# Kernel tuning notes

Measured on AMD Instinct MI355X. Metric: run time of the kernel, lower is better.

## Reference

```python
import jax, jax.numpy as jnp
import numpy as np

D_MODEL = 1024
D_STATE = 16
D_CONV = 4
EXPAND = 2
DT_RANK = 64
D_INNER = EXPAND * D_MODEL  # 2048
BATCH = 2
SEQ = 1024


def _silu(v):
    return v * jax.nn.sigmoid(v)


def setup_inputs() -> dict:
    key = jax.random.key(0)
    ks = jax.random.split(key, 8)
    x = jax.random.normal(ks[0], (BATCH, SEQ, D_MODEL), dtype=jnp.float32)
    W_in = jax.random.normal(ks[1], (2 * D_INNER, D_MODEL), dtype=jnp.float32) * (D_MODEL ** -0.5)
    conv_w = jax.random.normal(ks[2], (D_INNER, 1, D_CONV), dtype=jnp.float32) * (D_CONV ** -0.5)
    conv_b = jnp.zeros((D_INNER,), dtype=jnp.float32)
    W_x = jax.random.normal(ks[3], (DT_RANK + 2 * D_STATE, D_INNER), dtype=jnp.float32) * (D_INNER ** -0.5)
    W_dt = jax.random.uniform(ks[4], (D_INNER, DT_RANK), minval=-(DT_RANK ** -0.5), maxval=DT_RANK ** -0.5, dtype=jnp.float32)
    # dt bias init: inverse-softplus of dt sampled log-uniform in [1e-3, 1e-1]
    dt = jnp.exp(jax.random.uniform(ks[5], (D_INNER,), dtype=jnp.float32) * (np.log(0.1) - np.log(0.001)) + np.log(0.001))
    dt = jnp.clip(dt, 1e-4)
    b_dt = dt + jnp.log(-jnp.expm1(-dt))
    # A_log init: log of 1..d_state tiled per channel (S4D-real)
    A_log = jnp.log(jnp.tile(jnp.arange(1, D_STATE + 1, dtype=jnp.float32), (D_INNER, 1)))
    D = jnp.ones((D_INNER,), dtype=jnp.float32)
    W_out = jax.random.normal(ks[6], (D_MODEL, D_INNER), dtype=jnp.float32) * (D_INNER ** -0.5)
    return {"x": x, "W_in": W_in, "conv_w": conv_w, "conv_b": conv_b, "W_x": W_x,
            "W_dt": W_dt, "b_dt": b_dt, "A_log": A_log, "D": D, "W_out": W_out}


def _selective_scan(u, dt, A, B_in, C_in, D):
    # u, dt: [B,L,d_inner]; B_in, C_in: [B,L,d_state]; A: [d_inner,d_state]; D: [d_inner]
    Bsz = u.shape[0]

    def step(h, inp):
        u_t, dt_t, B_t, C_t = inp  # [B,d_inner], [B,d_inner], [B,d_state], [B,d_state]
        dA = jnp.exp(dt_t[:, :, None] * A)                     # [B,d_inner,d_state]
        h = dA * h + dt_t[:, :, None] * B_t[:, None, :] * u_t[:, :, None]
        y = jnp.einsum('bds,bs->bd', h, C_t)
        return h, y

    h0 = jnp.zeros((Bsz, D_INNER, D_STATE), dtype=u.dtype)
    xs = (u.transpose(1, 0, 2), dt.transpose(1, 0, 2),
          B_in.transpose(1, 0, 2), C_in.transpose(1, 0, 2))
    _, ys = jax.lax.scan(step, h0, xs)                          # ys: [L,B,d_inner]
    return ys.transpose(1, 0, 2) + u * D


def reference(x, W_in, conv_w, conv_b, W_x, W_dt, b_dt, A_log, D, W_out):
    # in_proj and gate split
    xz = x @ W_in.T                                            # [B,T,2*d_inner]
    x_in, z = jnp.split(xz, 2, axis=-1)
    # depthwise causal conv1d (left-pad d_conv-1, same as pad-both + slice :T)
    xi = x_in.transpose(0, 2, 1)                               # [B,d_inner,T]
    conv = jax.lax.conv_general_dilated(xi, conv_w, window_strides=(1,),
                                        padding=[(D_CONV - 1, 0)],
                                        feature_group_count=D_INNER)
    x_act = _silu(conv + conv_b[None, :, None]).transpose(0, 2, 1)  # [B,T,d_inner]
    # dt / B / C projections
    dbc = x_act @ W_x.T
    dt_lr, B_in, C_in = jnp.split(dbc, [DT_RANK, DT_RANK + D_STATE], axis=-1)
    dt = jax.nn.softplus(dt_lr @ W_dt.T + b_dt)                # [B,T,d_inner]
    A = -jnp.exp(A_log)                                        # [d_inner,d_state]
    y = _selective_scan(x_act, dt, A, B_in, C_in, D)
    y = y * _silu(z)
    return y @ W_out.T
```

## Files before the change

kernel.cpp:

```cpp
#include <hip/hip_runtime.h>
#include <math.h>

#define D_MODEL 1024
#define D_STATE 16
#define D_CONV  4
#define DT_RANK 64
#define D_INNER 2048
#define BATCH   2
#define SEQ     1024
#define BT      (BATCH*SEQ)
#define NCHUNK  32
#define CLEN    (SEQ/NCHUNK)
#define KSPLIT  16

typedef int   v4i __attribute__((ext_vector_type(4)));
typedef float v4f __attribute__((ext_vector_type(4)));
typedef unsigned short u16;

template<int BM, int BN, int BK, int TM, int TN, int EPI>
__launch_bounds__(256)
__global__ void gemm_nt(const float* __restrict__ A, int lda,
                        const float* __restrict__ B, int ldb,
                        float* __restrict__ C, int ldc,
                        int K, const float* __restrict__ bias) {
    constexpr int BX = BN / TN;
    constexpr int BY = BM / TM;
    constexpr int THREADS = BX * BY;

    __shared__ float As[BK][BM + 1];
    __shared__ float Bs[BK][BN + 1];

    const int tid = threadIdx.x;
    const int tx  = tid % BX;
    const int ty  = tid / BX;
    const int m0  = blockIdx.y * BM;
    const int n0  = blockIdx.x * BN;

    float acc[TM][TN] = {};

    for (int k0 = 0; k0 < K; k0 += BK) {
        #pragma unroll
        for (int l = 0; l < (BM * BK) / (THREADS * 4); ++l) {
            int idx = (tid + l * THREADS) * 4;
            int row = idx / BK, col = idx % BK;
            const float4 v = *reinterpret_cast<const float4*>(
                &A[(size_t)(m0 + row) * lda + k0 + col]);
            As[col + 0][row] = v.x; As[col + 1][row] = v.y;
            As[col + 2][row] = v.z; As[col + 3][row] = v.w;
        }
        #pragma unroll
        for (int l = 0; l < (BN * BK) / (THREADS * 4); ++l) {
            int idx = (tid + l * THREADS) * 4;
            int row = idx / BK, col = idx % BK;
            const float4 v = *reinterpret_cast<const float4*>(
                &B[(size_t)(n0 + row) * ldb + k0 + col]);
            Bs[col + 0][row] = v.x; Bs[col + 1][row] = v.y;
            Bs[col + 2][row] = v.z; Bs[col + 3][row] = v.w;
        }
        __syncthreads();

        #pragma unroll
        for (int kk = 0; kk < BK; ++kk) {
            float a[TM], b[TN];
            #pragma unroll
            for (int i = 0; i < TM; ++i) a[i] = As[kk][ty * TM + i];
            #pragma unroll
            for (int j = 0; j < TN; ++j) b[j] = Bs[kk][tx * TN + j];
            #pragma unroll
            for (int i = 0; i < TM; ++i)
                #pragma unroll
                for (int j = 0; j < TN; ++j)
                    acc[i][j] = fmaf(a[i], b[j], acc[i][j]);
        }
        __syncthreads();
    }

    #pragma unroll
    for (int i = 0; i < TM; ++i) {
        float* outp = &C[(size_t)(m0 + ty * TM + i) * ldc + n0 + tx * TN];
        float vals[4];
        #pragma unroll
        for (int j = 0; j < TN; ++j) {
            float val = acc[i][j];
            if (EPI == 1) {
                val += bias[n0 + tx * TN + j];
                val = (val > 20.f) ? val : log1pf(expf(val));
            }
            vals[j] = val;
        }
        float4 v;
        v.x = vals[0]; v.y = vals[1]; v.z = vals[2]; v.w = vals[3];
        *reinterpret_cast<float4*>(outp) = v;
    }
}

template<int BM, int BN, int BK, int TM, int TN>
__launch_bounds__(128)
__global__ void gemm_nt_splitk(const float* __restrict__ A, int lda,
                               const float* __restrict__ B, int ldb,
                               float* __restrict__ part, int N, int kchunk) {
    constexpr int BX = BN / TN;
    constexpr int BY = BM / TM;
    constexpr int THREADS = BX * BY;

    __shared__ float As[BK][BM + 1];
    __shared__ float Bs[BK][BN + 1];

    const int tid = threadIdx.x;
    const int tx  = tid % BX;
    const int ty  = tid / BX;
    const int m0  = blockIdx.y * BM;
    const int n0  = blockIdx.x * BN;
    const int kb  = blockIdx.z * kchunk;

    float acc[TM][TN] = {};

    for (int k0 = kb; k0 < kb + kchunk; k0 += BK) {
        #pragma unroll
        for (int l = 0; l < (BM * BK) / (THREADS * 4); ++l) {
            int idx = (tid + l * THREADS) * 4;
            int row = idx / BK, col = idx % BK;
            const float4 v = *reinterpret_cast<const float4*>(
                &A[(size_t)(m0 + row) * lda + k0 + col]);
            As[col + 0][row] = v.x; As[col + 1][row] = v.y;
            As[col + 2][row] = v.z; As[col + 3][row] = v.w;
        }
        #pragma unroll
        for (int l = 0; l < (BN * BK) / (THREADS * 4); ++l) {
            int idx = (tid + l * THREADS) * 4;
            int row = idx / BK, col = idx % BK;
            const float4 v = *reinterpret_cast<const float4*>(
                &B[(size_t)(n0 + row) * ldb + k0 + col]);
            Bs[col + 0][row] = v.x; Bs[col + 1][row] = v.y;
            Bs[col + 2][row] = v.z; Bs[col + 3][row] = v.w;
        }
        __syncthreads();

        #pragma unroll
        for (int kk = 0; kk < BK; ++kk) {
            float a[TM], b[TN];
            #pragma unroll
            for (int i = 0; i < TM; ++i) a[i] = As[kk][ty * TM + i];
            #pragma unroll
            for (int j = 0; j < TN; ++j) b[j] = Bs[kk][tx * TN + j];
            #pragma unroll
            for (int i = 0; i < TM; ++i)
                #pragma unroll
                for (int j = 0; j < TN; ++j)
                    acc[i][j] = fmaf(a[i], b[j], acc[i][j]);
        }
        __syncthreads();
    }

    float* base = part + (size_t)blockIdx.z * BT * N;
    #pragma unroll
    for (int i = 0; i < TM; ++i) {
        float* outp = &base[(size_t)(m0 + ty * TM + i) * N + n0 + tx * TN];
        float4 v;
        v.x = acc[i][0]; v.y = acc[i][1]; v.z = acc[i][2]; v.w = acc[i][3];
        *reinterpret_cast<float4*>(outp) = v;
    }
}

__global__ void reduce_splitk(const float* __restrict__ part,
                              float* __restrict__ outp, int n) {
    const int idx = blockIdx.x * 256 + threadIdx.x;
    if (idx >= n) return;
    float s = 0.f;
    #pragma unroll
    for (int kc = 0; kc < KSPLIT; ++kc)
        s += part[(size_t)kc * n + idx];
    outp[idx] = s;
}

__device__ __forceinline__ u16 rne_bf16(float x) {
    unsigned int u = __float_as_uint(x);
    unsigned int r = u + 0x7FFFu + ((u >> 16) & 1u);
    return (u16)(r >> 16);
}

__global__ void prep_kernel(const float* __restrict__ x,
                            const float* __restrict__ Win,
                            const float* __restrict__ Wout,
                            u16* __restrict__ xhi, u16* __restrict__ xlo,
                            u16* __restrict__ winh, u16* __restrict__ wouth) {
    const size_t M2 = 2u * 1024u * 1024u;
    size_t i = ((size_t)blockIdx.x * 256 + threadIdx.x) * 8;
    if (i < M2) {
        float4 a = *reinterpret_cast<const float4*>(&x[i]);
        float4 b = *reinterpret_cast<const float4*>(&x[i + 4]);
        float xs[8] = {a.x, a.y, a.z, a.w, b.x, b.y, b.z, b.w};
        unsigned int hw[4], lw[4];
        #pragma unroll
        for (int q = 0; q < 4; ++q) {
            u16 h0 = rne_bf16(xs[2*q]);
            u16 h1 = rne_bf16(xs[2*q+1]);
            float d0 = xs[2*q]   - __uint_as_float((unsigned int)h0 << 16);
            float d1 = xs[2*q+1] - __uint_as_float((unsigned int)h1 << 16);
            hw[q] = (unsigned int)h0 | ((unsigned int)h1 << 16);
            lw[q] = (unsigned int)rne_bf16(d0) | ((unsigned int)rne_bf16(d1) << 16);
        }
        *reinterpret_cast<v4i*>(&xhi[i]) = *reinterpret_cast<v4i*>(hw);
        *reinterpret_cast<v4i*>(&xlo[i]) = *reinterpret_cast<v4i*>(lw);
    } else if (i < 3 * M2) {
        size_t j = i - M2;
        float4 a = *reinterpret_cast<const float4*>(&Win[j]);
        float4 b = *reinterpret_cast<const float4*>(&Win[j + 4]);
        float xs[8] = {a.x, a.y, a.z, a.w, b.x, b.y, b.z, b.w};
        unsigned int hw[4];
        #pragma unroll
        for (int q = 0; q < 4; ++q)
            hw[q] = (unsigned int)rne_bf16(xs[2*q]) | ((unsigned int)rne_bf16(xs[2*q+1]) << 16);
        *reinterpret_cast<v4i*>(&winh[j]) = *reinterpret_cast<v4i*>(hw);
    } else {
        size_t j = i - 3 * M2;
        float4 a = *reinterpret_cast<const float4*>(&Wout[j]);
        float4 b = *reinterpret_cast<const float4*>(&Wout[j + 4]);
        float xs[8] = {a.x, a.y, a.z, a.w, b.x, b.y, b.z, b.w};
        unsigned int hw[4];
        #pragma unroll
        for (int q = 0; q < 4; ++q)
            hw[q] = (unsigned int)rne_bf16(xs[2*q]) | ((unsigned int)rne_bf16(xs[2*q+1]) << 16);
        *reinterpret_cast<v4i*>(&wouth[j]) = *reinterpret_cast<v4i*>(hw);
    }
}

#define MFMA_B16(ACC, Af, Bf) \
    asm("v_mfma_f32_16x16x32_bf16 %0, %1, %2, %0" : "+v"(ACC) : "v"(Af), "v"(Bf))

template<int BM, int BN, int WM, int WN>
__launch_bounds__(256)
__global__ void gemm_mfma2(const u16* __restrict__ Ahi, const u16* __restrict__ Alo, int lda,
                           const u16* __restrict__ Bhi, int ldb,
                           float* __restrict__ C, int ldc, int K) {
    constexpr int ACH = BM / 64;
    constexpr int BCH = BN / 64;
    constexpr int WMF = WM / 16;
    constexpr int WNF = WN / 16;
    constexpr int SA  = BM * 40;
    constexpr int SB  = BN * 40;
    constexpr int BUFSZ = 2 * SA + SB;
    constexpr int WCOLS = BN / WN;

    __shared__ u16 smem[2 * BUFSZ];

    const int tid  = threadIdx.x;
    const int lane = tid & 63;
    const int wave = tid >> 6;
    const int wr   = wave / WCOLS, wc = wave % WCOLS;
    const int m0   = blockIdx.y * BM, n0 = blockIdx.x * BN;

    size_t aBase[ACH]; int aW[ACH];
    #pragma unroll
    for (int q = 0; q < ACH; ++q) {
        int c = tid + q * 256, row = c >> 2, slot = c & 3;
        aBase[q] = (size_t)(m0 + row) * lda + slot * 8;
        aW[q] = row * 40 + slot * 8;
    }
    size_t bBase[BCH]; int bW[BCH];
    #pragma unroll
    for (int q = 0; q < BCH; ++q) {
        int c = tid + q * 256, row = c >> 2, slot = c & 3;
        bBase[q] = (size_t)(n0 + row) * ldb + slot * 8;
        bW[q] = row * 40 + slot * 8;
    }

    const int fr = lane & 15;
    const int fk = (lane >> 4) * 8;
    const int fq = lane >> 4;
    int aOff[WMF], bOff[WNF];
    #pragma unroll
    for (int i = 0; i < WMF; ++i) aOff[i] = (wr * WM + i * 16 + fr) * 40 + fk;
    #pragma unroll
    for (int j = 0; j < WNF; ++j) bOff[j] = (wc * WN + j * 16 + fr) * 40 + fk;

    v4f acc[WMF][WNF];
    #pragma unroll
    for (int i = 0; i < WMF; ++i)
        #pragma unroll
        for (int j = 0; j < WNF; ++j)
            acc[i][j] = (v4f)0.f;

    v4i rAh[ACH], rAl[ACH], rBh[BCH];
    #pragma unroll
    for (int q = 0; q < ACH; ++q) {
        rAh[q] = *reinterpret_cast<const v4i*>(Ahi + aBase[q]);
        rAl[q] = *reinterpret_cast<const v4i*>(Alo + aBase[q]);
    }
    #pragma unroll
    for (int q = 0; q < BCH; ++q)
        rBh[q] = *reinterpret_cast<const v4i*>(Bhi + bBase[q]);
    #pragma unroll
    for (int q = 0; q < ACH; ++q) {
        *reinterpret_cast<v4i*>(&smem[aW[q]]) = rAh[q];
        *reinterpret_cast<v4i*>(&smem[SA + aW[q]]) = rAl[q];
    }
    #pragma unroll
    for (int q = 0; q < BCH; ++q)
        *reinterpret_cast<v4i*>(&smem[2 * SA + bW[q]]) = rBh[q];
    __syncthreads();

    const int NK = K / 32;
    for (int k = 0; k < NK; ++k) {
        u16* sc = smem + (k & 1) * BUFSZ;
        if (k + 1 < NK) {
            const int k0 = (k + 1) * 32;
            #pragma unroll
            for (int q = 0; q < ACH; ++q) {
                rAh[q] = *reinterpret_cast<const v4i*>(Ahi + aBase[q] + k0);
                rAl[q] = *reinterpret_cast<const v4i*>(Alo + aBase[q] + k0);
            }
            #pragma unroll
            for (int q = 0; q < BCH; ++q)
                rBh[q] = *reinterpret_cast<const v4i*>(Bhi + bBase[q] + k0);
        }

        v4i ah[WMF], al[WMF];
        #pragma unroll
        for (int i = 0; i < WMF; ++i) {
            ah[i] = *reinterpret_cast<const v4i*>(&sc[aOff[i]]);
            al[i] = *reinterpret_cast<const v4i*>(&sc[SA + aOff[i]]);
        }
        #pragma unroll
        for (int j = 0; j < WNF; ++j) {
            v4i bh = *reinterpret_cast<const v4i*>(&sc[2 * SA + bOff[j]]);
            #pragma unroll
            for (int i = 0; i < WMF; ++i) {
                MFMA_B16(acc[i][j], ah[i], bh);
                MFMA_B16(acc[i][j], al[i], bh);
            }
        }

        if (k + 1 < NK) {
            u16* sn = smem + ((k + 1) & 1) * BUFSZ;
            #pragma unroll
            for (int q = 0; q < ACH; ++q) {
                *reinterpret_cast<v4i*>(&sn[aW[q]]) = rAh[q];
                *reinterpret_cast<v4i*>(&sn[SA + aW[q]]) = rAl[q];
            }
            #pragma unroll
            for (int q = 0; q < BCH; ++q)
                *reinterpret_cast<v4i*>(&sn[2 * SA + bW[q]]) = rBh[q];
            __syncthreads();
        }
    }

    asm volatile("s_nop 7\n\ts_nop 7\n\ts_nop 7" ::: "memory");

    #pragma unroll
    for (int i = 0; i < WMF; ++i) {
        const int row = m0 + wr * WM + i * 16 + fq * 4;
        #pragma unroll
        for (int j = 0; j < WNF; ++j) {
            const int col = n0 + wc * WN + j * 16 + fr;
            #pragma unroll
            for (int r = 0; r < 4; ++r)
                C[(size_t)(row + r) * ldc + col] = acc[i][j][r];
        }
    }
}

__global__ void conv_silu_kernel(const float* __restrict__ x_in, int xld,
                                 const float* __restrict__ w,
                                 const float* __restrict__ b,
                                 float* __restrict__ x_act) {
    const int idx = blockIdx.x * blockDim.x + threadIdx.x;
    const int ch = idx % D_INNER;
    const int m  = idx / D_INNER;
    const int t  = m % SEQ;

    float acc = b[ch];
    #pragma unroll
    for (int j = 0; j < D_CONV; ++j) {
        int tt = t - (D_CONV - 1) + j;
        if (tt >= 0)
            acc = fmaf(w[ch * D_CONV + j], x_in[(size_t)(m - (D_CONV - 1) + j) * xld + ch], acc);
    }
    x_act[idx] = acc / (1.f + __expf(-acc));
}

__launch_bounds__(256)
__global__ void scan_part1(const float* __restrict__ dt,
                           const float* __restrict__ x_act,
                           const float* __restrict__ dbc,
                           const float* __restrict__ A_log,
                           float* __restrict__ P, float* __restrict__ F) {
    __shared__ float Bsh[CLEN][D_STATE];
    const int tid = threadIdx.x;
    const int d = blockIdx.x * 256 + tid;
    const int c = blockIdx.y;
    const int b = blockIdx.z;
    const int mbase = b * SEQ + c * CLEN;

    {
        const int s = tid & 15, t0 = tid >> 4;
        #pragma unroll
        for (int q = 0; q < 2; ++q)
            Bsh[t0 + 16 * q][s] = dbc[(size_t)(mbase + t0 + 16 * q) * 96 + DT_RANK + s];
    }
    float A[16];
    #pragma unroll
    for (int q = 0; q < 4; ++q) {
        float4 v = *reinterpret_cast<const float4*>(&A_log[d * 16 + q * 4]);
        A[q*4+0] = -__expf(v.x); A[q*4+1] = -__expf(v.y);
        A[q*4+2] = -__expf(v.z); A[q*4+3] = -__expf(v.w);
    }
    __syncthreads();

    float h[16] = {};
    float Pp[16];
    #pragma unroll
    for (int s = 0; s < 16; ++s) Pp[s] = 1.f;

    for (int t = 0; t < CLEN; ++t) {
        const int m = mbase + t;
        const float dtv = dt[(size_t)m * D_INNER + d];
        const float u   = x_act[(size_t)m * D_INNER + d];
        const float du  = dtv * u;
        float Bv[16];
        #pragma unroll
        for (int q = 0; q < 4; ++q) {
            float4 v = *reinterpret_cast<const float4*>(&Bsh[t][q * 4]);
            Bv[q*4+0] = v.x; Bv[q*4+1] = v.y; Bv[q*4+2] = v.z; Bv[q*4+3] = v.w;
        }
        #pragma unroll
        for (int s = 0; s < 16; ++s) {
            const float dA = __expf(dtv * A[s]);
            Pp[s] *= dA;
            h[s] = fmaf(dA, h[s], du * Bv[s]);
        }
    }
    const size_t base = ((size_t)(b * NCHUNK + c) * 16) * D_INNER + d;
    #pragma unroll
    for (int s = 0; s < 16; ++s) {
        P[base + (size_t)s * D_INNER] = Pp[s];
        F[base + (size_t)s * D_INNER] = h[s];
    }
}

__launch_bounds__(256, 2)
__global__ void scan_combine(const float* __restrict__ P, float* F) {
    const int idx = blockIdx.x * 256 + threadIdx.x;
    const int d  = idx % D_INNER;
    const int bs = idx / D_INNER;
    const int b  = bs >> 4, s = bs & 15;
    const size_t base0 = ((size_t)b * NCHUNK * 16 + s) * D_INNER + d;
    const size_t cstep = (size_t)16 * D_INNER;

    float Pv[NCHUNK], Fv[NCHUNK];
    #pragma unroll
    for (int c = 0; c < NCHUNK; ++c) {
        Pv[c] = P[base0 + c * cstep];
        Fv[c] = F[base0 + c * cstep];
    }
    float G = 0.f;
    #pragma unroll
    for (int c = 0; c < NCHUNK; ++c) {
        const float f = Fv[c];
        Fv[c] = G;
        G = fmaf(Pv[c], G, f);
    }
    #pragma unroll
    for (int c = 0; c < NCHUNK; ++c)
        F[base0 + c * cstep] = Fv[c];
}

template<int BF16OUT>
__launch_bounds__(256)
__global__ void scan_part2(const float* __restrict__ dt,
                           const float* __restrict__ x_act,
                           const float* __restrict__ dbc,
                           const float* __restrict__ A_log,
                           const float* __restrict__ Dp,
                           const float* __restrict__ Ginit,
                           const float* zp, int zld,
                           float* yf, u16* yh, u16* yl) {
    __shared__ float BCs[CLEN][32];
    const int tid = threadIdx.x;
    const int d = blockIdx.x * 256 + tid;
    const int c = blockIdx.y;
    const int b = blockIdx.z;
    const int mbase = b * SEQ + c * CLEN;

    {
        const int t0 = tid >> 3;
        const int j  = (tid & 7) * 4;
        float4 v = *reinterpret_cast<const float4*>(
            &dbc[(size_t)(mbase + t0) * 96 + DT_RANK + j]);
        *reinterpret_cast<float4*>(&BCs[t0][j]) = v;
    }
    float A[16];
    #pragma unroll
    for (int q = 0; q < 4; ++q) {
        float4 v = *reinterpret_cast<const float4*>(&A_log[d * 16 + q * 4]);
        A[q*4+0] = -__expf(v.x); A[q*4+1] = -__expf(v.y);
        A[q*4+2] = -__expf(v.z); A[q*4+3] = -__expf(v.w);
    }
    float h[16];
    const size_t gbase = ((size_t)(b * NCHUNK + c) * 16) * D_INNER + d;
    #pragma unroll
    for (int s = 0; s < 16; ++s) h[s] = Ginit[gbase + (size_t)s * D_INNER];
    const float Dv = Dp[d];
    __syncthreads();

    for (int half = 0; half < 2; ++half) {
        const int tb = half * (CLEN / 2);
        float zreg[CLEN / 2];
        #pragma unroll
        for (int t = 0; t < CLEN / 2; ++t)
            zreg[t] = zp[(size_t)(mbase + tb + t) * zld + d];

        for (int t = 0; t < CLEN / 2; ++t) {
            const int m = mbase + tb + t;
            const float dtv = dt[(size_t)m * D_INNER + d];
            const float u   = x_act[(size_t)m * D_INNER + d];
            const float du  = dtv * u;
            float Bv[16], Cv[16];
            #pragma unroll
            for (int q = 0; q < 4; ++q) {
                float4 vb = *reinterpret_cast<const float4*>(&BCs[tb + t][q * 4]);
                float4 vc = *reinterpret_cast<const float4*>(&BCs[tb + t][16 + q * 4]);
                Bv[q*4+0] = vb.x; Bv[q*4+1] = vb.y; Bv[q*4+2] = vb.z; Bv[q*4+3] = vb.w;
                Cv[q*4+0] = vc.x; Cv[q*4+1] = vc.y; Cv[q*4+2] = vc.z; Cv[q*4+3] = vc.w;
            }
            float y0 = 0.f, y1 = 0.f;
            #pragma unroll
            for (int s = 0; s < 16; s += 2) {
                const float dA0 = __expf(dtv * A[s]);
                const float dA1 = __expf(dtv * A[s + 1]);
                h[s]     = fmaf(dA0, h[s],     du * Bv[s]);
                h[s + 1] = fmaf(dA1, h[s + 1], du * Bv[s + 1]);
                y0 = fmaf(h[s],     Cv[s],     y0);
                y1 = fmaf(h[s + 1], Cv[s + 1], y1);
            }
            float y = y0 + y1;
            y = fmaf(u, Dv, y);
            const float zv = zreg[t];
            const float g  = zv / (1.f + __expf(-zv));
            const float val = y * g;
            if (BF16OUT) {
                const u16 hh = rne_bf16(val);
                yh[(size_t)m * D_INNER + d] = hh;
                yl[(size_t)m * D_INNER + d] =
                    rne_bf16(val - __uint_as_float((unsigned int)hh << 16));
            } else {
                yf[(size_t)m * D_INNER + d] = val;
            }
        }
    }
}

extern "C" void kernel_launch(void* const* d_in, const int* in_sizes, int n_in,
                              void* d_out, int out_size, void* d_ws, size_t ws_size,
                              hipStream_t stream) {
    const float* x      = (const float*)d_in[0];
    const float* W_in   = (const float*)d_in[1];
    const float* conv_w = (const float*)d_in[2];
    const float* conv_b = (const float*)d_in[3];
    const float* W_x    = (const float*)d_in[4];
    const float* W_dt   = (const float*)d_in[5];
    const float* b_dt   = (const float*)d_in[6];
    const float* A_log  = (const float*)d_in[7];
    const float* Dp     = (const float*)d_in[8];
    const float* W_out  = (const float*)d_in[9];
    float* out = (float*)d_out;

    const size_t M1 = 1024u * 1024u;
    const size_t fXZ = 8 * M1, fXACT = 4 * M1, fDBC = (size_t)BT * 96,
                 fDT = 4 * M1;
    const size_t need = (fXZ + fXACT + fDBC + fDT) * 4 + 18 * M1 * 2;

    if (ws_size >= need) {
        float* ws    = (float*)d_ws;
        float* xz    = ws;
        float* x_act = xz    + fXZ;
        float* dbc   = x_act + fXACT;
        float* dtbuf = dbc   + fDBC;
        u16* xhi   = (u16*)(dtbuf + fDT);
        u16* xlo   = xhi   + 2 * M1;
        u16* winh  = xlo   + 2 * M1;
        u16* wouth = winh  + 4 * M1;
        u16* yh    = wouth + 2 * M1;
        u16* yl    = yh    + 4 * M1;
        float* Pbuf = (float*)xhi;
        float* Fbuf = (float*)winh;
        float* dbc_part = (float*)yh;

        prep_kernel<<<dim3((8 * M1) / 2048), 256, 0, stream>>>(
            x, W_in, W_out, xhi, xlo, winh, wouth);

        gemm_mfma2<128, 256, 64, 128><<<dim3(4096 / 256, BT / 128), 256, 0, stream>>>(
            xhi, xlo, D_MODEL, winh, D_MODEL, xz, 4096, D_MODEL);

        conv_silu_kernel<<<dim3((BT * D_INNER) / 256), 256, 0, stream>>>(
            xz, 4096, conv_w, conv_b, x_act);

        gemm_nt_splitk<64,32,16,4,4><<<dim3(96 / 32, BT / 64, KSPLIT), 128, 0, stream>>>(
            x_act, D_INNER, W_x, D_INNER, dbc_part, 96, D_INNER / KSPLIT);
        reduce_splitk<<<dim3((BT * 96 + 255) / 256), 256, 0, stream>>>(
            dbc_part, dbc, BT * 96);

        gemm_nt<64,64,16,4,4,1><<<dim3(D_INNER / 64, BT / 64), 256, 0, stream>>>(
            dbc, 96, W_dt, DT_RANK, dtbuf, D_INNER, DT_RANK, b_dt);

        scan_part1<<<dim3(D_INNER / 256, NCHUNK, BATCH), 256, 0, stream>>>(
            dtbuf, x_act, dbc, A_log, Pbuf, Fbuf);
        scan_combine<<<dim3((BATCH * 16 * D_INNER) / 256), 256, 0, stream>>>(
            Pbuf, Fbuf);
        scan_part2<1><<<dim3(D_INNER / 256, NCHUNK, BATCH), 256, 0, stream>>>(
            dtbuf, x_act, dbc, A_log, Dp, Fbuf, xz + D_INNER, 4096,
            nullptr, yh, yl);

        gemm_mfma2<64, 128, 32, 64><<<dim3(D_MODEL / 128, BT / 64), 256, 0, stream>>>(
            yh, yl, D_INNER, wouth, D_INNER, out, D_MODEL, D_INNER);
    } else {
        float* ws    = (float*)d_ws;
        float* x_in  = ws;
        float* z     = x_in  + (size_t)BT * D_INNER;
        float* x_act = z     + (size_t)BT * D_INNER;
        float* dbc   = x_act + (size_t)BT * D_INNER;
        float* Pbuf  = dbc   + (size_t)BT * 96;
        float* Fbuf  = Pbuf  + (size_t)BATCH * NCHUNK * 16 * D_INNER;
        float* dtbuf = x_in;
        float* yf    = z;

        gemm_nt<64,64,16,4,4,0><<<dim3(D_INNER/64, BT/64), 256, 0, stream>>>(
            x, D_MODEL, W_in, D_MODEL, x_in, D_INNER, D_MODEL, nullptr);
        gemm_nt<64,64,16,4,4,0><<<dim3(D_INNER/64, BT/64), 256, 0, stream>>>(
            x, D_MODEL, W_in + (size_t)D_INNER * D_MODEL, D_MODEL, z, D_INNER, D_MODEL, nullptr);
        conv_silu_kernel<<<dim3((BT * D_INNER) / 256), 256, 0, stream>>>(
            x_in, D_INNER, conv_w, conv_b, x_act);
        gemm_nt<64,32,16,4,4,0><<<dim3(96/32, BT/64), 128, 0, stream>>>(
            x_act, D_INNER, W_x, D_INNER, dbc, 96, D_INNER, nullptr);
        gemm_nt<64,64,16,4,4,1><<<dim3(D_INNER/64, BT/64), 256, 0, stream>>>(
            dbc, 96, W_dt, DT_RANK, dtbuf, D_INNER, DT_RANK, b_dt);
        scan_part1<<<dim3(D_INNER/256, NCHUNK, BATCH), 256, 0, stream>>>(
            dtbuf, x_act, dbc, A_log, Pbuf, Fbuf);
        scan_combine<<<dim3((BATCH * 16 * D_INNER) / 256), 256, 0, stream>>>(
            Pbuf, Fbuf);
        scan_part2<0><<<dim3(D_INNER/256, NCHUNK, BATCH), 256, 0, stream>>>(
            dtbuf, x_act, dbc, A_log, Dp, Fbuf, z, D_INNER, yf, nullptr, nullptr);
        gemm_nt<64,64,16,4,4,0><<<dim3(D_MODEL/64, BT/64), 256, 0, stream>>>(
            yf, D_INNER, W_out, D_INNER, out, D_MODEL, D_INNER, nullptr);
    }
}
```

Measured before the change: 220.8 us.

## Deepen MFMA GEMM prefetch pipeline and use compiler MFMA builtins

The bf16 split-precision MFMA GEMM now prefetches global tiles two K-steps ahead and writes the next LDS buffer before the current tile's math. Inline-asm MFMA is replaced by the __builtin_amdgcn_mfma_f32_16x16x32_bf16 intrinsic, so the compiler can schedule and insert hazards itself, and the trailing s_nop padding is removed. The MFMA ordering is also changed so hi and lo products into the same accumulator are separated by other MFMAs, reducing dependency stalls. The intent is better overlap of global loads, LDS writes and matrix math, at the cost of a sync every iteration and longer register lifetimes.

```diff
diff --git a/kernel.cpp b/kernel.cpp
--- a/kernel.cpp
+++ b/kernel.cpp
@@ -15,6 +15,7 @@
 
 typedef int   v4i __attribute__((ext_vector_type(4)));
 typedef float v4f __attribute__((ext_vector_type(4)));
+typedef short s8v __attribute__((ext_vector_type(8)));
 typedef unsigned short u16;
 
 template<int BM, int BN, int BK, int TM, int TN, int EPI>
@@ -224,9 +225,6 @@
         *reinterpret_cast<v4i*>(&wouth[j]) = *reinterpret_cast<v4i*>(hw);
     }
 }
-
-#define MFMA_B16(ACC, Af, Bf) \
-    asm("v_mfma_f32_16x16x32_bf16 %0, %1, %2, %0" : "+v"(ACC) : "v"(Af), "v"(Bf))
 
 template<int BM, int BN, int WM, int WN>
 __launch_bounds__(256)
@@ -282,70 +280,59 @@
             acc[i][j] = (v4f)0.f;
 
     v4i rAh[ACH], rAl[ACH], rBh[BCH];
-    #pragma unroll
-    for (int q = 0; q < ACH; ++q) {
-        rAh[q] = *reinterpret_cast<const v4i*>(Ahi + aBase[q]);
-        rAl[q] = *reinterpret_cast<const v4i*>(Alo + aBase[q]);
-    }
-    #pragma unroll
-    for (int q = 0; q < BCH; ++q)
-        rBh[q] = *reinterpret_cast<const v4i*>(Bhi + bBase[q]);
-    #pragma unroll
-    for (int q = 0; q < ACH; ++q) {
-        *reinterpret_cast<v4i*>(&smem[aW[q]]) = rAh[q];
-        *reinterpret_cast<v4i*>(&smem[SA + aW[q]]) = rAl[q];
-    }
-    #pragma unroll
-    for (int q = 0; q < BCH; ++q)
-        *reinterpret_cast<v4i*>(&smem[2 * SA + bW[q]]) = rBh[q];
+
+    auto loadg = [&](int k0) {
+        #pragma unroll
+        for (int q = 0; q < ACH; ++q) {
+            rAh[q] = *reinterpret_cast<const v4i*>(Ahi + aBase[q] + k0);
+            rAl[q] = *reinterpret_cast<const v4i*>(Alo + aBase[q] + k0);
+        }
+        #pragma unroll
+        for (int q = 0; q < BCH; ++q)
+            rBh[q] = *reinterpret_cast<const v4i*>(Bhi + bBase[q] + k0);
+    };
+    auto writelds = [&](u16* buf) {
+        #pragma unroll
+        for (int q = 0; q < ACH; ++q) {
+            *reinterpret_cast<v4i*>(&buf[aW[q]]) = rAh[q];
+            *reinterpret_cast<v4i*>(&buf[SA + aW[q]]) = rAl[q];
+        }
+        #pragma unroll
+        for (int q = 0; q < BCH; ++q)
+            *reinterpret_cast<v4i*>(&buf[2 * SA + bW[q]]) = rBh[q];
+    };
+
+    const int NK = K / 32;
+    loadg(0);
+    writelds(smem);
+    if (NK > 1) loadg(32);
     __syncthreads();
 
-    const int NK = K / 32;
     for (int k = 0; k < NK; ++k) {
-        u16* sc = smem + (k & 1) * BUFSZ;
+        u16* cur = smem + (k & 1) * BUFSZ;
         if (k + 1 < NK) {
-            const int k0 = (k + 1) * 32;
-            #pragma unroll
-            for (int q = 0; q < ACH; ++q) {
-                rAh[q] = *reinterpret_cast<const v4i*>(Ahi + aBase[q] + k0);
-                rAl[q] = *reinterpret_cast<const v4i*>(Alo + aBase[q] + k0);
-            }
-            #pragma unroll
-            for (int q = 0; q < BCH; ++q)
-                rBh[q] = *reinterpret_cast<const v4i*>(Bhi + bBase[q] + k0);
-        }
-
-        v4i ah[WMF], al[WMF];
+            writelds(smem + ((k + 1) & 1) * BUFSZ);
+            if (k + 2 < NK) loadg((k + 2) * 32);
+        }
+
+        s8v ah[WMF], al[WMF];
         #pragma unroll
         for (int i = 0; i < WMF; ++i) {
-            ah[i] = *reinterpret_cast<const v4i*>(&sc[aOff[i]]);
-            al[i] = *reinterpret_cast<const v4i*>(&sc[SA + aOff[i]]);
+            ah[i] = *reinterpret_cast<const s8v*>(&cur[aOff[i]]);
+            al[i] = *reinterpret_cast<const s8v*>(&cur[SA + aOff[i]]);
         }
         #pragma unroll
         for (int j = 0; j < WNF; ++j) {
-            v4i bh = *reinterpret_cast<const v4i*>(&sc[2 * SA + bOff[j]]);
-            #pragma unroll
-            for (int i = 0; i < WMF; ++i) {
-                MFMA_B16(acc[i][j], ah[i], bh);
-                MFMA_B16(acc[i][j], al[i], bh);
-            }
-        }
-
-        if (k + 1 < NK) {
-            u16* sn = smem + ((k + 1) & 1) * BUFSZ;
-            #pragma unroll
-            for (int q = 0; q < ACH; ++q) {
-                *reinterpret_cast<v4i*>(&sn[aW[q]]) = rAh[q];
-                *reinterpret_cast<v4i*>(&sn[SA + aW[q]]) = rAl[q];
-            }
-            #pragma unroll
-            for (int q = 0; q < BCH; ++q)
-                *reinterpret_cast<v4i*>(&sn[2 * SA + bW[q]]) = rBh[q];
-            __syncthreads();
-        }
-    }
-
-    asm volatile("s_nop 7\n\ts_nop 7\n\ts_nop 7" ::: "memory");
+            const s8v bh = *reinterpret_cast<const s8v*>(&cur[2 * SA + bOff[j]]);
+            #pragma unroll
+            for (int i = 0; i < WMF; ++i)
+                acc[i][j] = __builtin_amdgcn_mfma_f32_16x16x32_bf16(ah[i], bh, acc[i][j], 0, 0, 0);
+            #pragma unroll
+            for (int i = 0; i < WMF; ++i)
+                acc[i][j] = __builtin_amdgcn_mfma_f32_16x16x32_bf16(al[i], bh, acc[i][j], 0, 0, 0);
+        }
+        __syncthreads();
+    }
 
     #pragma unroll
     for (int i = 0; i < WMF; ++i) {
```

New measurement: 216.1 us. 2.1% less time.
